# Optimization experiments

Measured on AMD Instinct MI355X. Metric: run time of the kernel, lower is better.

## Reference

```python
import jax, jax.numpy as jnp
import numpy as np

NUM_USERS = 50000
NUM_ITEMS = 20000
N_NODES = NUM_USERS + NUM_ITEMS
D = 128
CONTENT_DIM = 512
BATCH = 8192
N_EDGES = 500000
NEG_SLOPE = 0.2  # GATConv leaky_relu slope


def setup_inputs() -> dict:
    key = jax.random.key(0)
    ks = jax.random.split(key, 16)
    return {
        "user_ids": jax.random.randint(ks[0], (BATCH,), 0, NUM_USERS),
        "item_ids": jax.random.randint(ks[1], (BATCH,), 0, NUM_ITEMS),
        "content_features": jax.random.normal(ks[2], (BATCH, CONTENT_DIM), jnp.float32),
        "edge_index": jax.random.randint(ks[3], (2, N_EDGES), 0, N_NODES),
        "user_emb_w": jax.random.normal(ks[4], (NUM_USERS, D), jnp.float32) * 0.05,
        "item_emb_w": jax.random.normal(ks[5], (NUM_ITEMS, D), jnp.float32) * 0.05,
        "content_proj_w": jax.random.normal(ks[6], (D, CONTENT_DIM), jnp.float32) * 0.04,
        "content_proj_b": jnp.zeros((D,), jnp.float32),
        "conv1_lin_w": jax.random.normal(ks[7], (2 * D, 2 * D), jnp.float32) * 0.06,
        "conv1_att_src": jax.random.normal(ks[8], (2, D), jnp.float32) * 0.1,
        "conv1_att_dst": jax.random.normal(ks[9], (2, D), jnp.float32) * 0.1,
        "conv1_bias": jnp.zeros((2 * D,), jnp.float32),
        "conv2_lin_w": jax.random.normal(ks[10], (D, 2 * D), jnp.float32) * 0.06,
        "conv2_att_src": jax.random.normal(ks[11], (1, D), jnp.float32) * 0.1,
        "conv2_att_dst": jax.random.normal(ks[12], (1, D), jnp.float32) * 0.1,
        "conv2_bias": jnp.zeros((D,), jnp.float32),
        "pred_w1": jax.random.normal(ks[13], (D, 3 * D), jnp.float32) * 0.05,
        "pred_b1": jnp.zeros((D,), jnp.float32),
        "pred_w2": jax.random.normal(ks[14], (1, D), jnp.float32) * 0.09,
        "pred_b2": jnp.zeros((1,), jnp.float32),
    }


def gat_conv(x, src, dst, lin_w, att_src, att_dst, bias, heads, out_ch):
    # PyG GATConv (shared lin for src/dst, concat=True, add_self_loops handled outside)
    n = x.shape[0]
    h = (x @ lin_w.T).reshape(n, heads, out_ch)          # [N,H,C]
    a_src = jnp.sum(h * att_src, axis=-1)                # [N,H]
    a_dst = jnp.sum(h * att_dst, axis=-1)                # [N,H]
    alpha = jax.nn.leaky_relu(a_src[src] + a_dst[dst], NEG_SLOPE)  # [E,H]
    # softmax over incoming edges of each destination node
    amax = jax.ops.segment_max(alpha, dst, num_segments=n)
    ex = jnp.exp(alpha - amax[dst])
    denom = jax.ops.segment_sum(ex, dst, num_segments=n)
    w = ex / denom[dst]                                  # [E,H]
    out = jax.ops.segment_sum(h[src] * w[:, :, None], dst, num_segments=n)
    return out.reshape(n, heads * out_ch) + bias


def _forward(user_ids, item_ids, edge_index, content_features, user_emb_w, item_emb_w,
             content_proj_w, content_proj_b, conv1_lin_w, conv1_att_src, conv1_att_dst,
             conv1_bias, conv2_lin_w, conv2_att_src, conv2_att_dst, conv2_bias,
             pred_w1, pred_b1, pred_w2, pred_b2):
    u_emb = user_emb_w[user_ids]                         # [B,D]
    i_emb = item_emb_w[item_ids]                         # [B,D]
    c_emb = content_features @ content_proj_w.T + content_proj_b  # [B,D]
    # scatter-init sparse node features (only batch nodes are nonzero, as in source)
    x = jnp.zeros((N_NODES, 2 * D), jnp.float32)
    x = x.at[user_ids].set(jnp.concatenate([u_emb, jnp.zeros_like(c_emb)], axis=1))
    x = x.at[NUM_USERS + item_ids].set(jnp.concatenate([i_emb, c_emb], axis=1))
    # add self loops (fill_value irrelevant: edge_weight unused by GATConv)
    loops = jnp.arange(N_NODES, dtype=edge_index.dtype)
    src = jnp.concatenate([edge_index[0], loops])
    dst = jnp.concatenate([edge_index[1], loops])
    x = jax.nn.elu(gat_conv(x, src, dst, conv1_lin_w, conv1_att_src, conv1_att_dst, conv1_bias, 2, D))
    # dropout inactive (eval mode)
    x = gat_conv(x, src, dst, conv2_lin_w, conv2_att_src, conv2_att_dst, conv2_bias, 1, D)
    combined = jnp.concatenate([u_emb, x[NUM_USERS + item_ids], x[user_ids]], axis=1)  # [B,3D]
    h = jax.nn.relu(combined @ pred_w1.T + pred_b1)
    return (h @ pred_w2.T + pred_b2).squeeze(-1)         # [B]


def reference(user_ids, item_ids, content_features, edge_index, user_emb_w, item_emb_w,
              content_proj_w, content_proj_b, conv1_lin_w, conv1_att_src, conv1_att_dst,
              conv1_bias, conv2_lin_w, conv2_att_src, conv2_att_dst, conv2_bias,
              pred_w1, pred_b1, pred_w2, pred_b2):
    return _forward(user_ids, item_ids, edge_index, content_features, user_emb_w, item_emb_w,
                    content_proj_w, content_proj_b, conv1_lin_w, conv1_att_src, conv1_att_dst,
                    conv1_bias, conv2_lin_w, conv2_att_src, conv2_att_dst, conv2_bias,
                    pred_w1, pred_b1, pred_w2, pred_b2)
```

## Files before the change

### kernel.cpp

```cpp
#include <hip/hip_runtime.h>
#include <hip/hip_bf16.h>

#define NU 50000
#define NI 20000
#define NN 70000
#define DD 128
#define BB 8192
#define EE 500000
#define ET 570000
#define NTASK 16384

__device__ __forceinline__ float lrelu(float x) { return x > 0.f ? x : 0.2f * x; }

typedef __attribute__((ext_vector_type(8))) short bf16x8;
typedef __attribute__((ext_vector_type(8))) unsigned short u16x8;
typedef __attribute__((ext_vector_type(4))) float f32x4;

__device__ __forceinline__ unsigned short f2bf_rne(float f) {
  unsigned int u = __builtin_bit_cast(unsigned int, f);
  u += 0x7FFFu + ((u >> 16) & 1u);
  return (unsigned short)(u >> 16);
}
__device__ __forceinline__ float bf2f(unsigned short h) {
  unsigned int u = ((unsigned int)h) << 16;
  return __builtin_bit_cast(float, u);
}

template <int GATHER, int MODE>
__global__ __launch_bounds__(256) void gemm_mfma(
    const float* __restrict__ A,
    const unsigned short* __restrict__ Bh, const unsigned short* __restrict__ Bl,
    const float* __restrict__ bias, float* __restrict__ C,
    unsigned short* __restrict__ Cb, int ldc,
    int M, int N, int K, int act,
    const int* __restrict__ idx0, const int* __restrict__ idx1,
    const int* __restrict__ mapv,
    const float* __restrict__ gA0, const float* __restrict__ gA1,
    const float* __restrict__ att_s, const float* __restrict__ att_d,
    float* __restrict__ a1s, float* __restrict__ a1d) {
  __shared__ __align__(16) unsigned short sAh[8][64][8];
  __shared__ __align__(16) unsigned short sAl[8][64][8];
  __shared__ __align__(16) unsigned short sBh[8][64][8];
  __shared__ __align__(16) unsigned short sBl[8][64][8];
  int tid = threadIdx.x;
  int bm = blockIdx.x * 64, bn = blockIdx.y * 64;
  int lane = tid & 63, w = tid >> 6;
  int wr = (w >> 1) * 32, wc = (w & 1) * 32;
  int fr = lane & 15, fk = lane >> 4;
  f32x4 acc[2][2] = {};

  for (int k0 = 0; k0 < K; k0 += 64) {
    __syncthreads();
#pragma unroll
    for (int t = 0; t < 2; t++) {
      int f = tid + t * 256;
      int row = f >> 3, kb = f & 7;
      int kg = k0 + kb * 8;
      const float* ap;
      if (GATHER == 1) {
        int sec = kg >> 7;
        int kc = kg & 127;
        int r = bm + row;
        if (sec == 0)      ap = &gA0[(size_t)idx0[r] * 128 + kc];
        else if (sec == 1) ap = &gA1[(size_t)mapv[NU + idx1[r]] * 128 + kc];
        else               ap = &gA1[(size_t)mapv[idx0[r]] * 128 + kc];
      } else if (GATHER == 2) {
        ap = &gA0[(size_t)idx0[bm + row] * K + kg];
      } else {
        ap = &A[(size_t)(bm + row) * K + kg];
      }
      float4 v0 = *reinterpret_cast<const float4*>(ap);
      float4 v1 = *reinterpret_cast<const float4*>(ap + 4);
      float vv[8] = {v0.x, v0.y, v0.z, v0.w, v1.x, v1.y, v1.z, v1.w};
      u16x8 hv, lv;
#pragma unroll
      for (int j = 0; j < 8; j++) {
        unsigned short hh = f2bf_rne(vv[j]);
        hv[j] = hh;
        lv[j] = (unsigned short)(__builtin_bit_cast(unsigned int, vv[j] - bf2f(hh)) >> 16);
      }
      *reinterpret_cast<u16x8*>(&sAh[kb][row][0]) = hv;
      *reinterpret_cast<u16x8*>(&sAl[kb][row][0]) = lv;
    }
#pragma unroll
    for (int t = 0; t < 2; t++) {
      int f = tid + t * 256;
      int row = f >> 3, kb = f & 7;
      int kg = k0 + kb * 8;
      *reinterpret_cast<u16x8*>(&sBh[kb][row][0]) =
          *reinterpret_cast<const u16x8*>(&Bh[(size_t)(bn + row) * K + kg]);
      *reinterpret_cast<u16x8*>(&sBl[kb][row][0]) =
          *reinterpret_cast<const u16x8*>(&Bl[(size_t)(bn + row) * K + kg]);
    }
    __syncthreads();
#pragma unroll
    for (int s = 0; s < 2; s++) {
      int kb = s * 4 + fk;
      bf16x8 ah0 = *reinterpret_cast<const bf16x8*>(&sAh[kb][wr + fr][0]);
      bf16x8 ah1 = *reinterpret_cast<const bf16x8*>(&sAh[kb][wr + 16 + fr][0]);
      bf16x8 al0 = *reinterpret_cast<const bf16x8*>(&sAl[kb][wr + fr][0]);
      bf16x8 al1 = *reinterpret_cast<const bf16x8*>(&sAl[kb][wr + 16 + fr][0]);
      bf16x8 bh0 = *reinterpret_cast<const bf16x8*>(&sBh[kb][wc + fr][0]);
      bf16x8 bh1 = *reinterpret_cast<const bf16x8*>(&sBh[kb][wc + 16 + fr][0]);
      bf16x8 bl0 = *reinterpret_cast<const bf16x8*>(&sBl[kb][wc + fr][0]);
      bf16x8 bl1 = *reinterpret_cast<const bf16x8*>(&sBl[kb][wc + 16 + fr][0]);
      acc[0][0] = __builtin_amdgcn_mfma_f32_16x16x32_bf16(al0, bh0, acc[0][0], 0, 0, 0);
      acc[0][0] = __builtin_amdgcn_mfma_f32_16x16x32_bf16(ah0, bl0, acc[0][0], 0, 0, 0);
      acc[0][0] = __builtin_amdgcn_mfma_f32_16x16x32_bf16(ah0, bh0, acc[0][0], 0, 0, 0);
      acc[0][1] = __builtin_amdgcn_mfma_f32_16x16x32_bf16(al0, bh1, acc[0][1], 0, 0, 0);
      acc[0][1] = __builtin_amdgcn_mfma_f32_16x16x32_bf16(ah0, bl1, acc[0][1], 0, 0, 0);
      acc[0][1] = __builtin_amdgcn_mfma_f32_16x16x32_bf16(ah0, bh1, acc[0][1], 0, 0, 0);
      acc[1][0] = __builtin_amdgcn_mfma_f32_16x16x32_bf16(al1, bh0, acc[1][0], 0, 0, 0);
      acc[1][0] = __builtin_amdgcn_mfma_f32_16x16x32_bf16(ah1, bl0, acc[1][0], 0, 0, 0);
      acc[1][0] = __builtin_amdgcn_mfma_f32_16x16x32_bf16(ah1, bh0, acc[1][0], 0, 0, 0);
      acc[1][1] = __builtin_amdgcn_mfma_f32_16x16x32_bf16(al1, bh1, acc[1][1], 0, 0, 0);
      acc[1][1] = __builtin_amdgcn_mfma_f32_16x16x32_bf16(ah1, bl1, acc[1][1], 0, 0, 0);
      acc[1][1] = __builtin_amdgcn_mfma_f32_16x16x32_bf16(ah1, bh1, acc[1][1], 0, 0, 0);
    }
  }
  if (MODE == 1) {
    int head = bn >> 7;
    float ps[2][4] = {{0.f}}, pd[2][4] = {{0.f}};
#pragma unroll
    for (int j = 0; j < 2; j++) {
      int col = bn + wc + j * 16 + fr;
      float asc = att_s[col], adc = att_d[col];
#pragma unroll
      for (int i = 0; i < 2; i++) {
#pragma unroll
        for (int r = 0; r < 4; r++) {
          float v = acc[i][j][r];
          ps[i][r] += v * asc;
          pd[i][r] += v * adc;
          Cb[(size_t)(bm + wr + i * 16 + fk * 4 + r) * ldc + col] = f2bf_rne(v);
        }
      }
    }
#pragma unroll
    for (int o = 1; o < 16; o <<= 1) {
#pragma unroll
      for (int i = 0; i < 2; i++)
#pragma unroll
        for (int r = 0; r < 4; r++) {
          ps[i][r] += __shfl_xor(ps[i][r], o);
          pd[i][r] += __shfl_xor(pd[i][r], o);
        }
    }
    if (fr == 0) {
#pragma unroll
      for (int i = 0; i < 2; i++) {
#pragma unroll
        for (int r = 0; r < 4; r++) {
          int t = bm + wr + i * 16 + fk * 4 + r;
          int v = (t < BB) ? idx0[t] : NU + idx1[t - BB];
          if (mapv[v] == t) {
            atomicAdd(&a1s[(size_t)v * 2 + head], ps[i][r]);
            atomicAdd(&a1d[(size_t)v * 2 + head], pd[i][r]);
          }
        }
      }
    }
    return;
  }
#pragma unroll
  for (int j = 0; j < 2; j++) {
    int col = bn + wc + j * 16 + fr;
    float bj = bias ? bias[col] : 0.f;
#pragma unroll
    for (int i = 0; i < 2; i++) {
#pragma unroll
      for (int r = 0; r < 4; r++) {
        int row = bm + wr + i * 16 + fk * 4 + r;
        float v = acc[i][j][r] + bj;
        if (act == 1) v = fmaxf(v, 0.f);
        C[(size_t)row * ldc + col] = v;
      }
    }
  }
}

#define EB 2227
#define SPLB 832
#define XAB 4096
__global__ __launch_bounds__(256) void setup_kernel(
    const int* __restrict__ ei, const int* __restrict__ uid, const int* __restrict__ iid,
    int* __restrict__ deg, int* __restrict__ winner,
    const float* __restrict__ wc, unsigned short* wch, unsigned short* wcl,
    const float* __restrict__ w1, unsigned short* w1h, unsigned short* w1l,
    const float* __restrict__ w2, unsigned short* w2h, unsigned short* w2l,
    const float* __restrict__ pw1, unsigned short* p1h, unsigned short* p1l,
    const float* __restrict__ uemb, const float* __restrict__ iemb,
    float* __restrict__ Xa, int* __restrict__ map) {
  int bid = blockIdx.x, tid = threadIdx.x;
  if (bid < EB) {
    int e = bid * 256 + tid;
    if (e < BB) atomicMax(&winner[iid[e]], e);
    if (e >= ET) return;
    int dst = (e < EE) ? ei[EE + e] : (e - EE);
    atomicAdd(&deg[dst], 1);
    return;
  }
  if (bid < EB + SPLB) {
    int i = (bid - EB) * 256 + tid;
    const float* w; unsigned short* h; unsigned short* l; int idx;
    if (i < 65536) { w = wc; h = wch; l = wcl; idx = i; }
    else if (i < 131072) { w = w1; h = w1h; l = w1l; idx = i - 65536; }
    else if (i < 163840) { w = w2; h = w2h; l = w2l; idx = i - 131072; }
    else { w = pw1; h = p1h; l = p1l; idx = i - 163840; }
    float f = w[idx];
    unsigned short hh = f2bf_rne(f);
    h[idx] = hh;
    l[idx] = (unsigned short)(__builtin_bit_cast(unsigned int, f - bf2f(hh)) >> 16);
    return;
  }
  int t = (bid - EB - SPLB) * 4 + (tid >> 6);
  int lane = tid & 63;
  int c4 = lane * 4;
  if (t < BB) {
    int u = uid[t];
    float4 v = make_float4(0.f, 0.f, 0.f, 0.f);
    if (c4 < DD) v = *reinterpret_cast<const float4*>(&uemb[(size_t)u * DD + c4]);
    *reinterpret_cast<float4*>(&Xa[(size_t)t * 256 + c4]) = v;
    if (lane == 0) map[u] = t;
  } else {
    int it = iid[t - BB];
    if (c4 < DD) {
      float4 v = *reinterpret_cast<const float4*>(&iemb[(size_t)it * DD + c4]);
      *reinterpret_cast<float4*>(&Xa[(size_t)t * 256 + c4]) = v;
    }
    if (lane == 0) map[NU + it] = t;
  }
}

__global__ void rowstart_kernel(const int* __restrict__ deg, const int* __restrict__ winner,
                                const int* __restrict__ iid,
                                int* __restrict__ rowstart, int* __restrict__ fill,
                                int* __restrict__ counter, int* __restrict__ widx,
                                const float* __restrict__ w2,
                                const float* __restrict__ att2s, const float* __restrict__ att2d,
                                float* __restrict__ qs, float* __restrict__ qd) {
  int blk = blockIdx.x;
  if (blk == (NN + 255) / 256) {
    int k = threadIdx.x;
    float s = 0.f, d = 0.f;
#pragma unroll 4
    for (int j = 0; j < DD; j++) {
      float w = w2[(size_t)j * 256 + k];
      s += att2s[j] * w;
      d += att2d[j] * w;
    }
    qs[k] = s;
    qd[k] = d;
    return;
  }
  int v = blk * 256 + threadIdx.x;
  if (v < BB) widx[v] = winner[iid[v]];
  if (v >= NN) return;
  int s = atomicAdd(counter, deg[v]);
  rowstart[v] = s;
  fill[v] = s;
}

__global__ void fill_mark_kernel(const int* __restrict__ ei, int* __restrict__ fill,
                                 int* __restrict__ col, const int* __restrict__ map,
                                 unsigned char* __restrict__ needed) {
  int e = blockIdx.x * 256 + threadIdx.x;
  if (e >= ET) return;
  int src, dst;
  if (e < EE) { src = ei[e]; dst = ei[EE + e]; }
  else { src = e - EE; dst = src; }
  int pos = atomicAdd(&fill[dst], 1);
  col[pos] = src;
  if (map[dst] >= 0) needed[src] = 1;
}

__global__ __launch_bounds__(256) void conv1_agg_kernel(
    const int* __restrict__ col, const int* __restrict__ rowstart,
    const int* __restrict__ deg, const unsigned short* __restrict__ Hb,
    const int* __restrict__ map, const unsigned char* __restrict__ needed,
    const float* __restrict__ a1s, const float* __restrict__ a1d,
    const float* __restrict__ bias,
    const float* __restrict__ qs, const float* __restrict__ qd,
    unsigned short* __restrict__ x1b, float* __restrict__ a2s, float* __restrict__ a2d) {
  int v = blockIdx.x * 4 + (threadIdx.x >> 6);
  int lane = threadIdx.x & 63;
  if (!needed[v]) return;
  int head = lane >> 5;
  int d = deg[v], s0 = rowstart[v];
  float2 adv = *reinterpret_cast<const float2*>(&a1d[(size_t)v * 2]);
  float4 acc = make_float4(0.f, 0.f, 0.f, 0.f);
  float den;
  if (d <= 64) {
    bool act = lane < d;
    int ci = act ? col[s0 + lane] : 0;
    float2 asv = make_float2(0.f, 0.f);
    int ri = -1;
    if (act) {
      asv = *reinterpret_cast<const float2*>(&a1s[(size_t)ci * 2]);
      ri = map[ci];
    }
    float al0 = act ? lrelu(asv.x + adv.x) : -1e30f;
    float al1 = act ? lrelu(asv.y + adv.y) : -1e30f;
    float m0 = al0, m1 = al1;
#pragma unroll
    for (int o = 1; o < 64; o <<= 1) {
      m0 = fmaxf(m0, __shfl_xor(m0, o));
      m1 = fmaxf(m1, __shfl_xor(m1, o));
    }
    float ex0 = act ? __expf(al0 - m0) : 0.f;
    float ex1 = act ? __expf(al1 - m1) : 0.f;
    float cs0 = ex0, cs1 = ex1;
#pragma unroll
    for (int o = 1; o < 64; o <<= 1) {
      cs0 += __shfl_xor(cs0, o);
      cs1 += __shfl_xor(cs1, o);
    }
    den = head ? cs1 : cs0;
    for (int i2 = 0; i2 < d; i2++) {
      int r = __shfl(ri, i2);
      if (r >= 0) {
        float e0 = __shfl(ex0, i2), e1 = __shfl(ex1, i2);
        float ex = head ? e1 : e0;
        ushort4 hv = *reinterpret_cast<const ushort4*>(&Hb[((size_t)r << 8) + (lane << 2)]);
        acc.x += ex * bf2f(hv.x); acc.y += ex * bf2f(hv.y);
        acc.z += ex * bf2f(hv.z); acc.w += ex * bf2f(hv.w);
      }
    }
  } else {
    float m0 = -1e30f, m1 = -1e30f, den0 = 0.f, den1 = 0.f;
    for (int c0 = 0; c0 < d; c0 += 64) {
      int i = c0 + lane;
      bool act = i < d;
      int ci = act ? col[s0 + i] : 0;
      float2 asv = make_float2(0.f, 0.f);
      int ri = -1;
      if (act) {
        asv = *reinterpret_cast<const float2*>(&a1s[(size_t)ci * 2]);
        ri = map[ci];
      }
      float al0 = act ? lrelu(asv.x + adv.x) : -1e30f;
      float al1 = act ? lrelu(asv.y + adv.y) : -1e30f;
      float cm0 = al0, cm1 = al1;
#pragma unroll
      for (int o = 1; o < 64; o <<= 1) {
        cm0 = fmaxf(cm0, __shfl_xor(cm0, o));
        cm1 = fmaxf(cm1, __shfl_xor(cm1, o));
      }
      float nm0 = fmaxf(m0, cm0), nm1 = fmaxf(m1, cm1);
      float ex0 = act ? __expf(al0 - nm0) : 0.f;
      float ex1 = act ? __expf(al1 - nm1) : 0.f;
      float s0f = __expf(m0 - nm0), s1f = __expf(m1 - nm1);
      float cs0 = ex0, cs1 = ex1;
#pragma unroll
      for (int o = 1; o < 64; o <<= 1) {
        cs0 += __shfl_xor(cs0, o);
        cs1 += __shfl_xor(cs1, o);
      }
      den0 = den0 * s0f + cs0;
      den1 = den1 * s1f + cs1;
      float sc = head ? s1f : s0f;
      acc.x *= sc; acc.y *= sc; acc.z *= sc; acc.w *= sc;
      int n = min(64, d - c0);
      for (int i2 = 0; i2 < n; i2++) {
        int r = __shfl(ri, i2);
        if (r >= 0) {
          float e0 = __shfl(ex0, i2), e1 = __shfl(ex1, i2);
          float ex = head ? e1 : e0;
          ushort4 hv = *reinterpret_cast<const ushort4*>(&Hb[((size_t)r << 8) + (lane << 2)]);
          acc.x += ex * bf2f(hv.x); acc.y += ex * bf2f(hv.y);
          acc.z += ex * bf2f(hv.z); acc.w += ex * bf2f(hv.w);
        }
      }
      m0 = nm0; m1 = nm1;
    }
    den = head ? den1 : den0;
  }
  float inv = 1.f / den;
  float4 b4 = *reinterpret_cast<const float4*>(&bias[lane << 2]);
  float4 o;
  o.x = fmaf(acc.x, inv, b4.x);
  o.y = fmaf(acc.y, inv, b4.y);
  o.z = fmaf(acc.z, inv, b4.z);
  o.w = fmaf(acc.w, inv, b4.w);
  o.x = o.x > 0.f ? o.x : __expf(o.x) - 1.f;
  o.y = o.y > 0.f ? o.y : __expf(o.y) - 1.f;
  o.z = o.z > 0.f ? o.z : __expf(o.z) - 1.f;
  o.w = o.w > 0.f ? o.w : __expf(o.w) - 1.f;
  ushort4 st;
  st.x = f2bf_rne(o.x); st.y = f2bf_rne(o.y);
  st.z = f2bf_rne(o.z); st.w = f2bf_rne(o.w);
  *reinterpret_cast<ushort4*>(&x1b[((size_t)v << 8) + (lane << 2)]) = st;
  float4 sv = *reinterpret_cast<const float4*>(&qs[lane << 2]);
  float4 dv = *reinterpret_cast<const float4*>(&qd[lane << 2]);
  float ps = o.x * sv.x + o.y * sv.y + o.z * sv.z + o.w * sv.w;
  float pd = o.x * dv.x + o.y * dv.y + o.z * dv.z + o.w * dv.w;
#pragma unroll
  for (int of = 1; of < 64; of <<= 1) { ps += __shfl_xor(ps, of); pd += __shfl_xor(pd, of); }
  if (lane == 0) { a2s[v] = ps; a2d[v] = pd; }
}

__global__ __launch_bounds__(256) void conv2_agg_kernel(
    const int* __restrict__ uid, const int* __restrict__ iid,
    const int* __restrict__ col, const int* __restrict__ rowstart,
    const int* __restrict__ deg, const int* __restrict__ map,
    const unsigned short* __restrict__ x1b,
    const float* __restrict__ a2s, const float* __restrict__ a2d,
    float* __restrict__ agg) {
  int t = blockIdx.x * 4 + (threadIdx.x >> 6);
  int lane = threadIdx.x & 63;
  int v = (t < BB) ? uid[t] : NU + iid[t - BB];
  if (map[v] != t) return;
  int d = deg[v], s0 = rowstart[v];
  float ad = a2d[v];
  float4 acc = make_float4(0.f, 0.f, 0.f, 0.f);
  float den;
  if (d <= 64) {
    bool act = lane < d;
    int ci = act ? col[s0 + lane] : 0;
    float as = act ? a2s[ci] : 0.f;
    float al = act ? lrelu(as + ad) : -1e30f;
    float m = al;
#pragma unroll
    for (int o = 1; o < 64; o <<= 1) m = fmaxf(m, __shfl_xor(m, o));
    float ex = act ? __expf(al - m) : 0.f;
    float cs = ex;
#pragma unroll
    for (int o = 1; o < 64; o <<= 1) cs += __shfl_xor(cs, o);
    den = cs;
    for (int i2 = 0; i2 < d; i2++) {
      int r = __shfl(ci, i2);
      float e = __shfl(ex, i2);
      ushort4 hv = *reinterpret_cast<const ushort4*>(&x1b[((size_t)r << 8) + (lane << 2)]);
      acc.x += e * bf2f(hv.x); acc.y += e * bf2f(hv.y);
      acc.z += e * bf2f(hv.z); acc.w += e * bf2f(hv.w);
    }
  } else {
    float m = -1e30f; den = 0.f;
    for (int c0 = 0; c0 < d; c0 += 64) {
      int i = c0 + lane;
      bool act = i < d;
      int ci = act ? col[s0 + i] : 0;
      float as = act ? a2s[ci] : 0.f;
      float al = act ? lrelu(as + ad) : -1e30f;
      float cm = al;
#pragma unroll
      for (int o = 1; o < 64; o <<= 1) cm = fmaxf(cm, __shfl_xor(cm, o));
      float nm = fmaxf(m, cm);
      float ex = act ? __expf(al - nm) : 0.f;
      float sf = __expf(m - nm);
      float cs = ex;
#pragma unroll
      for (int o = 1; o < 64; o <<= 1) cs += __shfl_xor(cs, o);
      den = den * sf + cs;
      acc.x *= sf; acc.y *= sf; acc.z *= sf; acc.w *= sf;
      int n = min(64, d - c0);
      for (int i2 = 0; i2 < n; i2++) {
        int r = __shfl(ci, i2);
        float e = __shfl(ex, i2);
        ushort4 hv = *reinterpret_cast<const ushort4*>(&x1b[((size_t)r << 8) + (lane << 2)]);
        acc.x += e * bf2f(hv.x); acc.y += e * bf2f(hv.y);
        acc.z += e * bf2f(hv.z); acc.w += e * bf2f(hv.w);
      }
      m = nm;
    }
  }
  float inv = 1.f / den;
  float4 o = make_float4(acc.x * inv, acc.y * inv, acc.z * inv, acc.w * inv);
  *reinterpret_cast<float4*>(&agg[((size_t)t << 8) + (lane << 2)]) = o;
}

__global__ __launch_bounds__(256) void final_kernel(
    const float* __restrict__ ph, const float* __restrict__ w2,
    const float* __restrict__ b2, float* __restrict__ out) {
  int b = blockIdx.x * 4 + (threadIdx.x >> 6);
  int lane = threadIdx.x & 63;
  float2 hv = *reinterpret_cast<const float2*>(&ph[((size_t)b << 7) + (lane << 1)]);
  float2 wv = *reinterpret_cast<const float2*>(&w2[lane << 1]);
  float s = hv.x * wv.x + hv.y * wv.y;
  for (int o = 1; o < 64; o <<= 1) s += __shfl_xor(s, o);
  if (lane == 0) out[b] = s + b2[0];
}

extern "C" void kernel_launch(void* const* d_in, const int* in_sizes, int n_in,
                              void* d_out, int out_size, void* d_ws, size_t ws_size,
                              hipStream_t stream) {
  const int* uid = (const int*)d_in[0];
  const int* iid = (const int*)d_in[1];
  const float* content = (const float*)d_in[2];
  const int* ei = (const int*)d_in[3];
  const float* uemb = (const float*)d_in[4];
  const float* iemb = (const float*)d_in[5];
  const float* wc = (const float*)d_in[6];
  const float* bc = (const float*)d_in[7];
  const float* w1 = (const float*)d_in[8];
  const float* att1s = (const float*)d_in[9];
  const float* att1d = (const float*)d_in[10];
  const float* b1 = (const float*)d_in[11];
  const float* w2 = (const float*)d_in[12];
  const float* att2s = (const float*)d_in[13];
  const float* att2d = (const float*)d_in[14];
  const float* b2c = (const float*)d_in[15];
  const float* pw1 = (const float*)d_in[16];
  const float* pb1 = (const float*)d_in[17];
  const float* pw2 = (const float*)d_in[18];
  const float* pb2 = (const float*)d_in[19];
  float* out = (float*)d_out;
  char* ws = (char*)d_ws;

  size_t off = 0;
  auto alloc = [&](size_t bytes) {
    size_t o = off;
    off += (bytes + 255) & ~(size_t)255;
    return o;
  };
  size_t o_winner  = alloc(NI * 4);
  size_t o_map     = alloc(NN * 4);
  size_t o_a1s     = alloc((size_t)NN * 2 * 4);
  size_t o_a1d     = alloc((size_t)NN * 2 * 4);
  size_t o_deg     = alloc(NN * 4);
  size_t o_rs      = alloc(NN * 4);
  size_t o_fill    = alloc(NN * 4);
  size_t o_cnt     = alloc(4);
  size_t o_needed  = alloc(NN);
  size_t o_col     = alloc((size_t)ET * 4);
  size_t o_a2s     = alloc(NN * 4);
  size_t o_a2d     = alloc(NN * 4);
  size_t o_qs      = alloc(256 * 4);
  size_t o_qd      = alloc(256 * 4);
  size_t o_widx    = alloc(BB * 4);
  size_t o_wch = alloc(65536 * 2),  o_wcl = alloc(65536 * 2);
  size_t o_w1h = alloc(65536 * 2),  o_w1l = alloc(65536 * 2);
  size_t o_w2h = alloc(32768 * 2),  o_w2l = alloc(32768 * 2);
  size_t o_p1h = alloc(49152 * 2),  o_p1l = alloc(49152 * 2);
  size_t o_r1    = alloc(16777216 + 8388608);
  size_t o_xa    = o_r1;
  size_t o_hb    = o_r1 + 16777216;
  size_t o_agg   = o_r1;
  size_t o_out2c = o_r1 + 16777216;
  size_t o_ph    = o_r1;
  size_t o_x1b   = alloc((size_t)NN * 256 * 2);
  (void)ws_size; (void)in_sizes; (void)n_in; (void)out_size;

  int*   winner = (int*)(ws + o_winner);
  int*   map    = (int*)(ws + o_map);
  float* a1s    = (float*)(ws + o_a1s);
  float* a1d    = (float*)(ws + o_a1d);
  int*   deg    = (int*)(ws + o_deg);
  int*   rs     = (int*)(ws + o_rs);
  int*   fill   = (int*)(ws + o_fill);
  int*   cnt    = (int*)(ws + o_cnt);
  unsigned char* needed = (unsigned char*)(ws + o_needed);
  int*   col    = (int*)(ws + o_col);
  float* a2s    = (float*)(ws + o_a2s);
  float* a2d    = (float*)(ws + o_a2d);
  float* qs     = (float*)(ws + o_qs);
  float* qd     = (float*)(ws + o_qd);
  int*   widx   = (int*)(ws + o_widx);
  unsigned short* wch = (unsigned short*)(ws + o_wch);
  unsigned short* wcl = (unsigned short*)(ws + o_wcl);
  unsigned short* w1h = (unsigned short*)(ws + o_w1h);
  unsigned short* w1l = (unsigned short*)(ws + o_w1l);
  unsigned short* w2h = (unsigned short*)(ws + o_w2h);
  unsigned short* w2l = (unsigned short*)(ws + o_w2l);
  unsigned short* p1h = (unsigned short*)(ws + o_p1h);
  unsigned short* p1l = (unsigned short*)(ws + o_p1l);
  float* Xa     = (float*)(ws + o_xa);
  unsigned short* Hb = (unsigned short*)(ws + o_hb);
  float* agg    = (float*)(ws + o_agg);
  float* out2c  = (float*)(ws + o_out2c);
  float* ph     = (float*)(ws + o_ph);
  unsigned short* x1b = (unsigned short*)(ws + o_x1b);

  hipMemsetAsync(ws + o_winner, 0xFF, o_map - o_winner + (size_t)NN * 4, stream);
  hipMemsetAsync(ws + o_a1s, 0, o_a1d - o_a1s + (size_t)NN * 2 * 4, stream);
  hipMemsetAsync(ws + o_deg, 0, o_needed - o_deg + NN, stream);

  setup_kernel<<<EB + SPLB + XAB, 256, 0, stream>>>(
      ei, uid, iid, deg, winner,
      wc, wch, wcl, w1, w1h, w1l, w2, w2h, w2l, pw1, p1h, p1l,
      uemb, iemb, Xa, map);
  rowstart_kernel<<<(NN + 255) / 256 + 1, 256, 0, stream>>>(
      deg, winner, iid, rs, fill, cnt, widx, w2, att2s, att2d, qs, qd);
  {
    dim3 g(BB / 64, DD / 64);
    gemm_mfma<2, 0><<<g, 256, 0, stream>>>(
        nullptr, wch, wcl, bc, Xa + (size_t)BB * 256 + 128, nullptr, 256,
        BB, DD, 512, 0, widx, nullptr, nullptr, content, nullptr,
        nullptr, nullptr, nullptr, nullptr);
  }
  fill_mark_kernel<<<(ET + 255) / 256, 256, 0, stream>>>(ei, fill, col, map, needed);
  {
    dim3 g(NTASK / 64, 256 / 64);
    gemm_mfma<0, 1><<<g, 256, 0, stream>>>(
        Xa, w1h, w1l, nullptr, nullptr, Hb, 256,
        NTASK, 256, 256, 0, uid, iid, map, nullptr, nullptr,
        att1s, att1d, a1s, a1d);
  }
  conv1_agg_kernel<<<NN / 4, 256, 0, stream>>>(col, rs, deg, Hb, map, needed,
                                               a1s, a1d, b1, qs, qd, x1b, a2s, a2d);
  conv2_agg_kernel<<<NTASK / 4, 256, 0, stream>>>(uid, iid, col, rs, deg, map,
                                                  x1b, a2s, a2d, agg);
  {
    dim3 g(NTASK / 64, DD / 64);
    gemm_mfma<0, 0><<<g, 256, 0, stream>>>(
        agg, w2h, w2l, b2c, out2c, nullptr, 128,
        NTASK, DD, 256, 0, nullptr, nullptr, nullptr, nullptr, nullptr,
        nullptr, nullptr, nullptr, nullptr);
  }
  {
    dim3 g(BB / 64, DD / 64);
    gemm_mfma<1, 0><<<g, 256, 0, stream>>>(
        nullptr, p1h, p1l, pb1, ph, nullptr, 128,
        BB, DD, 384, 1, uid, iid, map, uemb, out2c,
        nullptr, nullptr, nullptr, nullptr);
  }
  final_kernel<<<BB / 4, 256, 0, stream>>>(ph, pw2, pb2, out);
}
```

Measured before the change: 220.5 us.

## Fuse content GEMM with CSR fill, fold final dot into predictor GEMM epilogue

Merges the content-projection GEMM and the edge fill/mark pass into one launch with disjoint block ranges so they can run concurrently. Adds an epilogue mode to the predictor GEMM that applies relu, dots with pred_w2 and atomically accumulates into the zeroed output, which removes the intermediate ph buffer and the final kernel. The conv1 aggregation now iterates only over neighbors that have a row, using a ballot mask instead of a per-edge branch. Atomic float accumulation makes the output order-dependent, and the extra memset adds a small cost.

```diff
diff --git a/kernel.cpp b/kernel.cpp
--- a/kernel.cpp
+++ b/kernel.cpp
@@ -27,7 +27,8 @@
 }
 
 template <int GATHER, int MODE>
-__global__ __launch_bounds__(256) void gemm_mfma(
+__device__ __forceinline__ void gemm_core(
+    int bm, int bn,
     const float* __restrict__ A,
     const unsigned short* __restrict__ Bh, const unsigned short* __restrict__ Bl,
     const float* __restrict__ bias, float* __restrict__ C,
@@ -43,7 +44,6 @@
   __shared__ __align__(16) unsigned short sBh[8][64][8];
   __shared__ __align__(16) unsigned short sBl[8][64][8];
   int tid = threadIdx.x;
-  int bm = blockIdx.x * 64, bn = blockIdx.y * 64;
   int lane = tid & 63, w = tid >> 6;
   int wr = (w >> 1) * 32, wc = (w & 1) * 32;
   int fr = lane & 15, fk = lane >> 4;
@@ -162,6 +162,43 @@
     }
     return;
   }
+  if (MODE == 2) {
+    float part[2][4] = {{0.f}};
+#pragma unroll
+    for (int j = 0; j < 2; j++) {
+      int col = bn + wc + j * 16 + fr;
+      float bj = bias[col];
+      float wv = att_s[col];
+#pragma unroll
+      for (int i = 0; i < 2; i++) {
+#pragma unroll
+        for (int r = 0; r < 4; r++) {
+          float v = fmaxf(acc[i][j][r] + bj, 0.f);
+          part[i][r] += v * wv;
+        }
+      }
+    }
+#pragma unroll
+    for (int o = 1; o < 16; o <<= 1) {
+#pragma unroll
+      for (int i = 0; i < 2; i++)
+#pragma unroll
+        for (int r = 0; r < 4; r++) part[i][r] += __shfl_xor(part[i][r], o);
+    }
+    if (fr == 0) {
+#pragma unroll
+      for (int i = 0; i < 2; i++) {
+#pragma unroll
+        for (int r = 0; r < 4; r++) {
+          int row = bm + wr + i * 16 + fk * 4 + r;
+          float add = part[i][r];
+          if (bn == 0 && wc == 0) add += att_d[0];
+          atomicAdd(&a1s[row], add);
+        }
+      }
+    }
+    return;
+  }
 #pragma unroll
   for (int j = 0; j < 2; j++) {
     int col = bn + wc + j * 16 + fr;
@@ -177,6 +214,48 @@
       }
     }
   }
+}
+
+template <int GATHER, int MODE>
+__global__ __launch_bounds__(256) void gemm_mfma(
+    const float* __restrict__ A,
+    const unsigned short* __restrict__ Bh, const unsigned short* __restrict__ Bl,
+    const float* __restrict__ bias, float* __restrict__ C,
+    unsigned short* __restrict__ Cb, int ldc,
+    int M, int N, int K, int act,
+    const int* __restrict__ idx0, const int* __restrict__ idx1,
+    const int* __restrict__ mapv,
+    const float* __restrict__ gA0, const float* __restrict__ gA1,
+    const float* __restrict__ att_s, const float* __restrict__ att_d,
+    float* __restrict__ a1s, float* __restrict__ a1d) {
+  gemm_core<GATHER, MODE>(blockIdx.x * 64, blockIdx.y * 64,
+                          A, Bh, Bl, bias, C, Cb, ldc, M, N, K, act,
+                          idx0, idx1, mapv, gA0, gA1, att_s, att_d, a1s, a1d);
+}
+
+#define GEMMB 256
+__global__ __launch_bounds__(256) void cembfill_kernel(
+    const unsigned short* __restrict__ wch, const unsigned short* __restrict__ wcl,
+    const float* __restrict__ bc, float* __restrict__ XaC,
+    const int* __restrict__ widx, const float* __restrict__ content,
+    const int* __restrict__ ei, int* __restrict__ fill, int* __restrict__ col,
+    const int* __restrict__ mapv, unsigned char* __restrict__ needed) {
+  int bid = blockIdx.x;
+  if (bid < GEMMB) {
+    gemm_core<2, 0>((bid >> 1) * 64, (bid & 1) * 64,
+                    nullptr, wch, wcl, bc, XaC, nullptr, 256,
+                    BB, DD, 512, 0, widx, nullptr, nullptr, content, nullptr,
+                    nullptr, nullptr, nullptr, nullptr);
+    return;
+  }
+  int e = (bid - GEMMB) * 256 + threadIdx.x;
+  if (e >= ET) return;
+  int src, dst;
+  if (e < EE) { src = ei[e]; dst = ei[EE + e]; }
+  else { src = e - EE; dst = src; }
+  int pos = atomicAdd(&fill[dst], 1);
+  col[pos] = src;
+  if (mapv[dst] >= 0) needed[src] = 1;
 }
 
 #define EB 2227
@@ -261,19 +340,6 @@
   fill[v] = s;
 }
 
-__global__ void fill_mark_kernel(const int* __restrict__ ei, int* __restrict__ fill,
-                                 int* __restrict__ col, const int* __restrict__ map,
-                                 unsigned char* __restrict__ needed) {
-  int e = blockIdx.x * 256 + threadIdx.x;
-  if (e >= ET) return;
-  int src, dst;
-  if (e < EE) { src = ei[e]; dst = ei[EE + e]; }
-  else { src = e - EE; dst = src; }
-  int pos = atomicAdd(&fill[dst], 1);
-  col[pos] = src;
-  if (map[dst] >= 0) needed[src] = 1;
-}
-
 __global__ __launch_bounds__(256) void conv1_agg_kernel(
     const int* __restrict__ col, const int* __restrict__ rowstart,
     const int* __restrict__ deg, const unsigned short* __restrict__ Hb,
@@ -290,6 +356,7 @@
   float2 adv = *reinterpret_cast<const float2*>(&a1d[(size_t)v * 2]);
   float4 acc = make_float4(0.f, 0.f, 0.f, 0.f);
   float den;
+  const unsigned short* hb = Hb + (lane << 2);
   if (d <= 64) {
     bool act = lane < d;
     int ci = act ? col[s0 + lane] : 0;
@@ -316,15 +383,16 @@
       cs1 += __shfl_xor(cs1, o);
     }
     den = head ? cs1 : cs0;
-    for (int i2 = 0; i2 < d; i2++) {
-      int r = __shfl(ri, i2);
-      if (r >= 0) {
-        float e0 = __shfl(ex0, i2), e1 = __shfl(ex1, i2);
-        float ex = head ? e1 : e0;
-        ushort4 hv = *reinterpret_cast<const ushort4*>(&Hb[((size_t)r << 8) + (lane << 2)]);
-        acc.x += ex * bf2f(hv.x); acc.y += ex * bf2f(hv.y);
-        acc.z += ex * bf2f(hv.z); acc.w += ex * bf2f(hv.w);
-      }
+    unsigned long long msk = __ballot(act && ri >= 0);
+    while (msk) {
+      int s = __ffsll((unsigned long long)msk) - 1;
+      msk &= msk - 1;
+      int r = __shfl(ri, s);
+      float e0 = __shfl(ex0, s), e1 = __shfl(ex1, s);
+      float ex = head ? e1 : e0;
+      ushort4 hv = *reinterpret_cast<const ushort4*>(&hb[(size_t)r << 8]);
+      acc.x += ex * bf2f(hv.x); acc.y += ex * bf2f(hv.y);
+      acc.z += ex * bf2f(hv.z); acc.w += ex * bf2f(hv.w);
     }
   } else {
     float m0 = -1e30f, m1 = -1e30f, den0 = 0.f, den1 = 0.f;
@@ -360,16 +428,16 @@
       den1 = den1 * s1f + cs1;
       float sc = head ? s1f : s0f;
       acc.x *= sc; acc.y *= sc; acc.z *= sc; acc.w *= sc;
-      int n = min(64, d - c0);
-      for (int i2 = 0; i2 < n; i2++) {
-        int r = __shfl(ri, i2);
-        if (r >= 0) {
-          float e0 = __shfl(ex0, i2), e1 = __shfl(ex1, i2);
-          float ex = head ? e1 : e0;
-          ushort4 hv = *reinterpret_cast<const ushort4*>(&Hb[((size_t)r << 8) + (lane << 2)]);
-          acc.x += ex * bf2f(hv.x); acc.y += ex * bf2f(hv.y);
-          acc.z += ex * bf2f(hv.z); acc.w += ex * bf2f(hv.w);
-        }
+      unsigned long long msk = __ballot(act && ri >= 0);
+      while (msk) {
+        int s = __ffsll((unsigned long long)msk) - 1;
+        msk &= msk - 1;
+        int r = __shfl(ri, s);
+        float e0 = __shfl(ex0, s), e1 = __shfl(ex1, s);
+        float ex = head ? e1 : e0;
+        ushort4 hv = *reinterpret_cast<const ushort4*>(&hb[(size_t)r << 8]);
+        acc.x += ex * bf2f(hv.x); acc.y += ex * bf2f(hv.y);
+        acc.z += ex * bf2f(hv.z); acc.w += ex * bf2f(hv.w);
       }
       m0 = nm0; m1 = nm1;
     }
@@ -414,6 +482,7 @@
   float ad = a2d[v];
   float4 acc = make_float4(0.f, 0.f, 0.f, 0.f);
   float den;
+  const unsigned short* xb = x1b + (lane << 2);
   if (d <= 64) {
     bool act = lane < d;
     int ci = act ? col[s0 + lane] : 0;
@@ -430,7 +499,7 @@
     for (int i2 = 0; i2 < d; i2++) {
       int r = __shfl(ci, i2);
       float e = __shfl(ex, i2);
-      ushort4 hv = *reinterpret_cast<const ushort4*>(&x1b[((size_t)r << 8) + (lane << 2)]);
+      ushort4 hv = *reinterpret_cast<const ushort4*>(&xb[(size_t)r << 8]);
       acc.x += e * bf2f(hv.x); acc.y += e * bf2f(hv.y);
       acc.z += e * bf2f(hv.z); acc.w += e * bf2f(hv.w);
     }
@@ -457,7 +526,7 @@
       for (int i2 = 0; i2 < n; i2++) {
         int r = __shfl(ci, i2);
         float e = __shfl(ex, i2);
-        ushort4 hv = *reinterpret_cast<const ushort4*>(&x1b[((size_t)r << 8) + (lane << 2)]);
+        ushort4 hv = *reinterpret_cast<const ushort4*>(&xb[(size_t)r << 8]);
         acc.x += e * bf2f(hv.x); acc.y += e * bf2f(hv.y);
         acc.z += e * bf2f(hv.z); acc.w += e * bf2f(hv.w);
       }
@@ -467,18 +536,6 @@
   float inv = 1.f / den;
   float4 o = make_float4(acc.x * inv, acc.y * inv, acc.z * inv, acc.w * inv);
   *reinterpret_cast<float4*>(&agg[((size_t)t << 8) + (lane << 2)]) = o;
-}
-
-__global__ __launch_bounds__(256) void final_kernel(
-    const float* __restrict__ ph, const float* __restrict__ w2,
-    const float* __restrict__ b2, float* __restrict__ out) {
-  int b = blockIdx.x * 4 + (threadIdx.x >> 6);
-  int lane = threadIdx.x & 63;
-  float2 hv = *reinterpret_cast<const float2*>(&ph[((size_t)b << 7) + (lane << 1)]);
-  float2 wv = *reinterpret_cast<const float2*>(&w2[lane << 1]);
-  float s = hv.x * wv.x + hv.y * wv.y;
-  for (int o = 1; o < 64; o <<= 1) s += __shfl_xor(s, o);
-  if (lane == 0) out[b] = s + b2[0];
 }
 
 extern "C" void kernel_launch(void* const* d_in, const int* in_sizes, int n_in,
@@ -537,7 +594,6 @@
   size_t o_hb    = o_r1 + 16777216;
   size_t o_agg   = o_r1;
   size_t o_out2c = o_r1 + 16777216;
-  size_t o_ph    = o_r1;
   size_t o_x1b   = alloc((size_t)NN * 256 * 2);
   (void)ws_size; (void)in_sizes; (void)n_in; (void)out_size;
 
@@ -568,12 +624,12 @@
   unsigned short* Hb = (unsigned short*)(ws + o_hb);
   float* agg    = (float*)(ws + o_agg);
   float* out2c  = (float*)(ws + o_out2c);
-  float* ph     = (float*)(ws + o_ph);
   unsigned short* x1b = (unsigned short*)(ws + o_x1b);
 
   hipMemsetAsync(ws + o_winner, 0xFF, o_map - o_winner + (size_t)NN * 4, stream);
   hipMemsetAsync(ws + o_a1s, 0, o_a1d - o_a1s + (size_t)NN * 2 * 4, stream);
   hipMemsetAsync(ws + o_deg, 0, o_needed - o_deg + NN, stream);
+  hipMemsetAsync(out, 0, BB * 4, stream);
 
   setup_kernel<<<EB + SPLB + XAB, 256, 0, stream>>>(
       ei, uid, iid, deg, winner,
@@ -581,14 +637,9 @@
       uemb, iemb, Xa, map);
   rowstart_kernel<<<(NN + 255) / 256 + 1, 256, 0, stream>>>(
       deg, winner, iid, rs, fill, cnt, widx, w2, att2s, att2d, qs, qd);
-  {
-    dim3 g(BB / 64, DD / 64);
-    gemm_mfma<2, 0><<<g, 256, 0, stream>>>(
-        nullptr, wch, wcl, bc, Xa + (size_t)BB * 256 + 128, nullptr, 256,
-        BB, DD, 512, 0, widx, nullptr, nullptr, content, nullptr,
-        nullptr, nullptr, nullptr, nullptr);
-  }
-  fill_mark_kernel<<<(ET + 255) / 256, 256, 0, stream>>>(ei, fill, col, map, needed);
+  cembfill_kernel<<<GEMMB + EB, 256, 0, stream>>>(
+      wch, wcl, bc, Xa + (size_t)BB * 256 + 128, widx, content,
+      ei, fill, col, map, needed);
   {
     dim3 g(NTASK / 64, 256 / 64);
     gemm_mfma<0, 1><<<g, 256, 0, stream>>>(
@@ -609,10 +660,9 @@
   }
   {
     dim3 g(BB / 64, DD / 64);
-    gemm_mfma<1, 0><<<g, 256, 0, stream>>>(
-        nullptr, p1h, p1l, pb1, ph, nullptr, 128,
-        BB, DD, 384, 1, uid, iid, map, uemb, out2c,
-        nullptr, nullptr, nullptr, nullptr);
-  }
-  final_kernel<<<BB / 4, 256, 0, stream>>>(ph, pw2, pb2, out);
-}
+    gemm_mfma<1, 2><<<g, 256, 0, stream>>>(
+        nullptr, p1h, p1l, pb1, nullptr, nullptr, 128,
+        BB, DD, 384, 0, uid, iid, map, uemb, out2c,
+        pw2, pb2, out, nullptr);
+  }
+}
```

New measurement: 205.8 us. -6.7%, faster.
